# Optimization experiments

Hardware: AMD Instinct MI355X
Metric: run time of the kernel (lower is better)

Reference implementation:

```python
import jax, jax.numpy as jnp
import numpy as np


def setup_inputs() -> dict:
    key = jax.random.key(0)
    k1, k2 = jax.random.split(key)
    B, H, N, D = 4, 16, 2048, 64
    x = jax.random.normal(k1, (B, H, N, D), dtype=jnp.float32)
    wqkv = 0.02 * jax.random.normal(k2, (H, D, 3 * D), dtype=jnp.float32)
    bqkv = jnp.zeros((H, 1, 3 * D), dtype=jnp.float32)
    return {"x": x, "wqkv": wqkv, "bqkv": bqkv}


def reference(x, wqkv, bqkv):
    # x: [B, H, N, D]; wqkv: [H, D, 3D]; bqkv: [H, 1, 3D]
    B, H, N, D = x.shape
    scale = D ** (-0.5)
    qkv = jnp.einsum('bhnd,hde->bhne', x, wqkv) + bqkv  # [B,H,N,3D]
    # Faithful to torch: reshape (3D,) -> (D, 3) then unbind last axis,
    # i.e. q/k/v are interleaved (stride-3) columns of the projection.
    qkv = qkv.reshape(B, H, N, D, 3)
    q = qkv[..., 0] * scale
    k = qkv[..., 1]
    v = qkv[..., 2]
    attn = jnp.einsum('bhqd,bhkd->bhqk', q, k)  # [B,H,N,N]
    attn = jax.nn.softmax(attn, axis=-1)
    out = jnp.einsum('bhqk,bhkd->bhqd', attn, v)  # [B,H,N,D]
    return out
```

## Files before the change

kernel.cpp:

```cpp
#include <hip/hip_runtime.h>
#include <hip/hip_bf16.h>
#include <stdint.h>

typedef short bf16x8 __attribute__((ext_vector_type(8)));
typedef short bf16x4 __attribute__((ext_vector_type(4)));
typedef float f32x4 __attribute__((ext_vector_type(4)));

#define BHC 64
#define NQ 2048
#define DD 64
#define NE 192
#define LDP 72
#define QSCALE 0.1803368801111245f

__device__ __forceinline__ short f2bf(float f) {
  unsigned u = __float_as_uint(f);
  unsigned r = (u + 0x7FFFu + ((u >> 16) & 1u)) >> 16;
  return (short)r;
}

__device__ __forceinline__ bf16x8 pack8(float4 a, float4 b) {
  bf16x8 v;
  v[0] = f2bf(a.x); v[1] = f2bf(a.y); v[2] = f2bf(a.z); v[3] = f2bf(a.w);
  v[4] = f2bf(b.x); v[5] = f2bf(b.y); v[6] = f2bf(b.z); v[7] = f2bf(b.w);
  return v;
}

__device__ __forceinline__ short2 pk_bf16(float a, float b) {
  __hip_bfloat162 c = __float22bfloat162_rn(make_float2(a, b));
  return *reinterpret_cast<short2*>(&c);
}

__global__ __launch_bounds__(256) void wprep_kernel(
    const float* __restrict__ w, const float* __restrict__ bq,
    short* __restrict__ wp, float* __restrict__ biasp) {
  const int h = blockIdx.y;
  const int r = blockIdx.x * 256 + threadIdx.x;
  const int j = r & 7;
  const int t = r >> 3;
  const int quad = t & 3, col = (t >> 2) & 15;
  const int kc = (t >> 6) & 1, ntb = (t >> 7) & 3, wh = t >> 9;
  const int d = kc * 32 + quad * 8 + j;
  const int e = (ntb * 16 + col) * 3 + wh;
  wp[h * 12288 + r] = f2bf(w[((size_t)h * DD + d) * NE + e]);
  if (r < 192) {
    const int wh2 = r / 64, c = r - wh2 * 64;
    biasp[h * 192 + r] = bq[h * NE + c * 3 + wh2];
  }
}

__global__ __launch_bounds__(256, 4) void proj_kernel(
    const float* __restrict__ x, const short* __restrict__ wp,
    const float* __restrict__ biasp, short* __restrict__ Qg,
    short* __restrict__ Kg, short* __restrict__ Vtg) {
  __shared__ short sV[4][64 * 24];

  const int tid = threadIdx.x;
  const int bh = blockIdx.x >> 5;
  const int rb = blockIdx.x & 31;
  const int h = bh & 15;
  const int wave = tid >> 6;
  const int lane = tid & 63;
  const int col = lane & 15, quad = lane >> 4;
  const int row0 = rb * 64 + wave * 16;

  const float* xrow = x + ((size_t)bh * NQ + row0 + col) * DD;
  bf16x8 aq[2];
#pragma unroll
  for (int kc = 0; kc < 2; ++kc) {
    const float4* p4 = (const float4*)(xrow + kc * 32 + quad * 8);
    aq[kc] = pack8(p4[0], p4[1]);
  }

  const short* wph = wp + h * 12288;
  const int fo = (col * 4 + quad) * 8;

  f32x4 acc[12];
#pragma unroll
  for (int nt = 0; nt < 12; ++nt) acc[nt] = (f32x4){0.f, 0.f, 0.f, 0.f};

#pragma unroll
  for (int nt = 0; nt < 12; ++nt) {
    bf16x8 bw0 = *(const bf16x8*)(wph + (nt * 2 + 0) * 512 + fo);
    bf16x8 bw1 = *(const bf16x8*)(wph + (nt * 2 + 1) * 512 + fo);
    acc[nt] = __builtin_amdgcn_mfma_f32_16x16x32_bf16(bw0, aq[0], acc[nt], 0, 0, 0);
    acc[nt] = __builtin_amdgcn_mfma_f32_16x16x32_bf16(bw1, aq[1], acc[nt], 0, 0, 0);
  }

  const float* bph = biasp + h * 192;
  short* Qp = Qg + ((size_t)bh * NQ + row0 + col) * DD;
  short* Kp = Kg + ((size_t)bh * NQ + row0 + col) * DD;
  short* sVw = sV[wave];

#pragma unroll
  for (int nt = 0; nt < 12; ++nt) {
    const int wh = nt >> 2, ntb = nt & 3;
    const float4 b4 = *(const float4*)(bph + wh * 64 + ntb * 16 + quad * 4);
    float v0 = acc[nt][0] + b4.x, v1 = acc[nt][1] + b4.y;
    float v2 = acc[nt][2] + b4.z, v3 = acc[nt][3] + b4.w;
    if (nt < 4) { v0 *= QSCALE; v1 *= QSCALE; v2 *= QSCALE; v3 *= QSCALE; }
    if (nt < 8) {
      short2 s01 = pk_bf16(v0, v1);
      short2 s23 = pk_bf16(v2, v3);
      bf16x4 pv; pv[0] = s01.x; pv[1] = s01.y; pv[2] = s23.x; pv[3] = s23.y;
      short* P = (nt < 4) ? Qp : Kp;
      *(bf16x4*)(P + ntb * 16 + quad * 4) = pv;
    } else {
      const int dd = ntb * 16 + quad * 4;
      sVw[(dd + 0) * 24 + col] = f2bf(v0);
      sVw[(dd + 1) * 24 + col] = f2bf(v1);
      sVw[(dd + 2) * 24 + col] = f2bf(v2);
      sVw[(dd + 3) * 24 + col] = f2bf(v3);
    }
  }

  short* Vp = Vtg + (size_t)bh * DD * NQ + row0;
#pragma unroll
  for (int c = 0; c < 2; ++c) {
    int idx = c * 64 + lane;
    int d = idx >> 1, half = (idx & 1) * 8;
    *(bf16x8*)(Vp + (size_t)d * NQ + half) = *(const bf16x8*)(sVw + d * 24 + half);
  }
}

__global__ __launch_bounds__(256, 2) void attn_kernel(
    const short* __restrict__ Qg, const short* __restrict__ Kg,
    const short* __restrict__ Vtg, float* __restrict__ out) {
  __shared__ short kbuf[2][64 * 64];
  __shared__ short vbuf[2][64 * 64];
  __shared__ short pbuf[4][64 * LDP];

  const int tid = threadIdx.x;
  const int bh = blockIdx.x & 63;
  const int qb = blockIdx.x >> 6;
  const int wave = tid >> 6, lane = tid & 63;
  const int col = lane & 15, quad = lane >> 4;
  const int qbase = qb * 256 + wave * 64;

  bf16x8 bqf[4][2];
#pragma unroll
  for (int ntq = 0; ntq < 4; ++ntq)
#pragma unroll
    for (int kc = 0; kc < 2; ++kc)
      bqf[ntq][kc] = *(const bf16x8*)(Qg + ((size_t)bh * NQ + qbase + ntq * 16 + col) * DD +
                                      kc * 32 + quad * 8);

  f32x4 o[4][4];
  float l_acc[4];
#pragma unroll
  for (int mtq = 0; mtq < 4; ++mtq) {
    l_acc[mtq] = 0.f;
#pragma unroll
    for (int ntd = 0; ntd < 4; ++ntd) o[mtq][ntd] = (f32x4){0.f, 0.f, 0.f, 0.f};
  }

  short* pb = pbuf[wave];
  const short* Kb = Kg + (size_t)bh * NQ * DD;
  const short* Vb = Vtg + (size_t)bh * DD * NQ;

  const int r0 = tid >> 3, c0 = tid & 7;
  const int dst0 = r0 * 64 + ((c0 ^ (r0 & 7)) * 8);
  const int dst1 = (r0 + 32) * 64 + ((c0 ^ (r0 & 7)) * 8);
  const int src0 = r0 * DD + c0 * 8;
  const size_t vsrc0o = (size_t)r0 * NQ + c0 * 8;
  const size_t vsrc1o = (size_t)(r0 + 32) * NQ + c0 * 8;

  {
    bf16x8 k0 = *(const bf16x8*)(Kb + src0);
    bf16x8 k1 = *(const bf16x8*)(Kb + src0 + 32 * DD);
    bf16x8 v0 = *(const bf16x8*)(Vb + vsrc0o);
    bf16x8 v1 = *(const bf16x8*)(Vb + vsrc1o);
    *(bf16x8*)(&kbuf[0][dst0]) = k0;
    *(bf16x8*)(&kbuf[0][dst1]) = k1;
    *(bf16x8*)(&vbuf[0][dst0]) = v0;
    *(bf16x8*)(&vbuf[0][dst1]) = v1;
  }
  __syncthreads();

#pragma unroll 1
  for (int t = 0; t < 32; ++t) {
    const int p = t & 1;
    const short* kb = kbuf[p];
    const short* vb_s = vbuf[p];

    bf16x8 nk0, nk1, nv0, nv1;
    if (t < 31) {
      const short* Kn = Kb + (t + 1) * 64 * DD;
      const short* Vn = Vb + (t + 1) * 64;
      nk0 = *(const bf16x8*)(Kn + src0);
      nk1 = *(const bf16x8*)(Kn + src0 + 32 * DD);
      nv0 = *(const bf16x8*)(Vn + vsrc0o);
      nv1 = *(const bf16x8*)(Vn + vsrc1o);
    }

#pragma unroll
    for (int mtk = 0; mtk < 4; ++mtk) {
      const int krow = mtk * 16 + col;
      const int kx = krow & 7;
      bf16x8 ka0 = *(const bf16x8*)(&kb[krow * 64 + ((quad ^ kx) * 8)]);
      bf16x8 ka1 = *(const bf16x8*)(&kb[krow * 64 + (((4 + quad) ^ kx) * 8)]);
#pragma unroll
      for (int ntq = 0; ntq < 4; ++ntq) {
        f32x4 s = (f32x4){0.f, 0.f, 0.f, 0.f};
        s = __builtin_amdgcn_mfma_f32_16x16x32_bf16(ka0, bqf[ntq][0], s, 0, 0, 0);
        s = __builtin_amdgcn_mfma_f32_16x16x32_bf16(ka1, bqf[ntq][1], s, 0, 0, 0);
        float p0 = __builtin_amdgcn_exp2f(s[0]);
        float p1 = __builtin_amdgcn_exp2f(s[1]);
        float p2 = __builtin_amdgcn_exp2f(s[2]);
        float p3 = __builtin_amdgcn_exp2f(s[3]);
        l_acc[ntq] += (p0 + p1) + (p2 + p3);
        short2 s01 = pk_bf16(p0, p1);
        short2 s23 = pk_bf16(p2, p3);
        bf16x4 pv; pv[0] = s01.x; pv[1] = s01.y; pv[2] = s23.x; pv[3] = s23.y;
        *(bf16x4*)(&pb[(ntq * 16 + col) * LDP + mtk * 16 + quad * 4]) = pv;
      }
    }

#pragma unroll
    for (int mtq = 0; mtq < 4; ++mtq) {
      bf16x8 ap0 = *(const bf16x8*)(&pb[(mtq * 16 + col) * LDP + quad * 8]);
      bf16x8 ap1 = *(const bf16x8*)(&pb[(mtq * 16 + col) * LDP + 32 + quad * 8]);
#pragma unroll
      for (int ntd = 0; ntd < 4; ++ntd) {
        const int vrow = ntd * 16 + col;
        const int vx = vrow & 7;
        bf16x8 vf0 = *(const bf16x8*)(&vb_s[vrow * 64 + ((quad ^ vx) * 8)]);
        bf16x8 vf1 = *(const bf16x8*)(&vb_s[vrow * 64 + (((4 + quad) ^ vx) * 8)]);
        o[mtq][ntd] = __builtin_amdgcn_mfma_f32_16x16x32_bf16(ap0, vf0, o[mtq][ntd], 0, 0, 0);
        o[mtq][ntd] = __builtin_amdgcn_mfma_f32_16x16x32_bf16(ap1, vf1, o[mtq][ntd], 0, 0, 0);
      }
    }

    if (t < 31) {
      short* kn = kbuf[1 - p];
      short* vn = vbuf[1 - p];
      *(bf16x8*)(&kn[dst0]) = nk0;
      *(bf16x8*)(&kn[dst1]) = nk1;
      *(bf16x8*)(&vn[dst0]) = nv0;
      *(bf16x8*)(&vn[dst1]) = nv1;
      __syncthreads();
    }
  }

#pragma unroll
  for (int mtq = 0; mtq < 4; ++mtq) {
    float l = l_acc[mtq];
    l += __shfl_xor(l, 16);
    l += __shfl_xor(l, 32);
#pragma unroll
    for (int r = 0; r < 4; ++r) {
      float inv = 1.0f / __shfl(l, quad * 4 + r);
      int rq = qbase + mtq * 16 + quad * 4 + r;
      float* orow = out + ((size_t)bh * NQ + rq) * DD;
#pragma unroll
      for (int ntd = 0; ntd < 4; ++ntd) orow[ntd * 16 + col] = o[mtq][ntd][r] * inv;
    }
  }
}

extern "C" void kernel_launch(void* const* d_in, const int* in_sizes, int n_in,
                              void* d_out, int out_size, void* d_ws, size_t ws_size,
                              hipStream_t stream) {
  const float* x = (const float*)d_in[0];
  const float* w = (const float*)d_in[1];
  const float* bq = (const float*)d_in[2];
  float* out = (float*)d_out;

  short* Qg = (short*)d_ws;
  short* Kg = Qg + (size_t)BHC * NQ * DD;
  short* Vtg = Kg + (size_t)BHC * NQ * DD;
  short* wp = Vtg + (size_t)BHC * DD * NQ;
  float* biasp = (float*)(wp + 16 * 12288);

  wprep_kernel<<<dim3(48, 16), dim3(256), 0, stream>>>(w, bq, wp, biasp);
  proj_kernel<<<dim3(2048), dim3(256), 0, stream>>>(x, wp, biasp, Qg, Kg, Vtg);
  attn_kernel<<<dim3(512), dim3(256), 0, stream>>>(Qg, Kg, Vtg, out);
}
```

Before: 183.8 us.

## Hold projection weights in registers and loop each wave over four row tiles

The projection kernel now loads all 24 weight fragments into registers once per wave and reuses them across four 16-row tiles, so each wave covers 64 rows and the grid shrinks from 2048 to 512 blocks. The next tile's x rows are prefetched while the current tile's MFMAs run, and the bias is used as the initial accumulator. V is transposed through a wider shared tile so Vt stores are full 64-row contiguous chunks. This cuts repeated weight loads and per-block overhead, but raises register pressure and removes the occupancy hint from the launch bounds.

```diff
diff --git a/kernel.cpp b/kernel.cpp
--- a/kernel.cpp
+++ b/kernel.cpp
@@ -49,77 +49,95 @@
   }
 }
 
-__global__ __launch_bounds__(256, 4) void proj_kernel(
+__global__ __launch_bounds__(256) void proj_kernel(
     const float* __restrict__ x, const short* __restrict__ wp,
     const float* __restrict__ biasp, short* __restrict__ Qg,
     short* __restrict__ Kg, short* __restrict__ Vtg) {
-  __shared__ short sV[4][64 * 24];
+  __shared__ short sV[4][64 * 72];
 
   const int tid = threadIdx.x;
-  const int bh = blockIdx.x >> 5;
-  const int rb = blockIdx.x & 31;
+  const int bh = blockIdx.x >> 3;
+  const int rb = blockIdx.x & 7;
   const int h = bh & 15;
   const int wave = tid >> 6;
   const int lane = tid & 63;
   const int col = lane & 15, quad = lane >> 4;
-  const int row0 = rb * 64 + wave * 16;
-
-  const float* xrow = x + ((size_t)bh * NQ + row0 + col) * DD;
-  bf16x8 aq[2];
-#pragma unroll
-  for (int kc = 0; kc < 2; ++kc) {
-    const float4* p4 = (const float4*)(xrow + kc * 32 + quad * 8);
-    aq[kc] = pack8(p4[0], p4[1]);
-  }
+  const int wbase = rb * 256 + wave * 64;
 
   const short* wph = wp + h * 12288;
   const int fo = (col * 4 + quad) * 8;
-
-  f32x4 acc[12];
-#pragma unroll
-  for (int nt = 0; nt < 12; ++nt) acc[nt] = (f32x4){0.f, 0.f, 0.f, 0.f};
-
-#pragma unroll
-  for (int nt = 0; nt < 12; ++nt) {
-    bf16x8 bw0 = *(const bf16x8*)(wph + (nt * 2 + 0) * 512 + fo);
-    bf16x8 bw1 = *(const bf16x8*)(wph + (nt * 2 + 1) * 512 + fo);
-    acc[nt] = __builtin_amdgcn_mfma_f32_16x16x32_bf16(bw0, aq[0], acc[nt], 0, 0, 0);
-    acc[nt] = __builtin_amdgcn_mfma_f32_16x16x32_bf16(bw1, aq[1], acc[nt], 0, 0, 0);
-  }
+  bf16x8 wf[24];
+#pragma unroll
+  for (int i = 0; i < 24; ++i) wf[i] = *(const bf16x8*)(wph + i * 512 + fo);
 
   const float* bph = biasp + h * 192;
-  short* Qp = Qg + ((size_t)bh * NQ + row0 + col) * DD;
-  short* Kp = Kg + ((size_t)bh * NQ + row0 + col) * DD;
+  const float* xb = x + ((size_t)bh * NQ + wbase + col) * DD;
   short* sVw = sV[wave];
 
-#pragma unroll
-  for (int nt = 0; nt < 12; ++nt) {
-    const int wh = nt >> 2, ntb = nt & 3;
-    const float4 b4 = *(const float4*)(bph + wh * 64 + ntb * 16 + quad * 4);
-    float v0 = acc[nt][0] + b4.x, v1 = acc[nt][1] + b4.y;
-    float v2 = acc[nt][2] + b4.z, v3 = acc[nt][3] + b4.w;
-    if (nt < 4) { v0 *= QSCALE; v1 *= QSCALE; v2 *= QSCALE; v3 *= QSCALE; }
-    if (nt < 8) {
-      short2 s01 = pk_bf16(v0, v1);
-      short2 s23 = pk_bf16(v2, v3);
-      bf16x4 pv; pv[0] = s01.x; pv[1] = s01.y; pv[2] = s23.x; pv[3] = s23.y;
-      short* P = (nt < 4) ? Qp : Kp;
-      *(bf16x4*)(P + ntb * 16 + quad * 4) = pv;
-    } else {
-      const int dd = ntb * 16 + quad * 4;
-      sVw[(dd + 0) * 24 + col] = f2bf(v0);
-      sVw[(dd + 1) * 24 + col] = f2bf(v1);
-      sVw[(dd + 2) * 24 + col] = f2bf(v2);
-      sVw[(dd + 3) * 24 + col] = f2bf(v3);
-    }
-  }
-
-  short* Vp = Vtg + (size_t)bh * DD * NQ + row0;
-#pragma unroll
-  for (int c = 0; c < 2; ++c) {
-    int idx = c * 64 + lane;
-    int d = idx >> 1, half = (idx & 1) * 8;
-    *(bf16x8*)(Vp + (size_t)d * NQ + half) = *(const bf16x8*)(sVw + d * 24 + half);
+  bf16x8 aqc[2];
+#pragma unroll
+  for (int kc = 0; kc < 2; ++kc) {
+    const float4* p4 = (const float4*)(xb + kc * 32 + quad * 8);
+    aqc[kc] = pack8(p4[0], p4[1]);
+  }
+
+#pragma unroll
+  for (int r = 0; r < 4; ++r) {
+    float4 nx0, nx1, nx2, nx3;
+    if (r < 3) {
+      const float* xn = xb + (size_t)(r + 1) * 16 * DD;
+      nx0 = *(const float4*)(xn + quad * 8);
+      nx1 = *(const float4*)(xn + quad * 8 + 4);
+      nx2 = *(const float4*)(xn + 32 + quad * 8);
+      nx3 = *(const float4*)(xn + 32 + quad * 8 + 4);
+    }
+
+    f32x4 acc[12];
+#pragma unroll
+    for (int nt = 0; nt < 12; ++nt)
+      acc[nt] = *(const f32x4*)(bph + (nt >> 2) * 64 + (nt & 3) * 16 + quad * 4);
+
+#pragma unroll
+    for (int nt = 0; nt < 12; ++nt) {
+      acc[nt] = __builtin_amdgcn_mfma_f32_16x16x32_bf16(wf[nt * 2 + 0], aqc[0], acc[nt], 0, 0, 0);
+      acc[nt] = __builtin_amdgcn_mfma_f32_16x16x32_bf16(wf[nt * 2 + 1], aqc[1], acc[nt], 0, 0, 0);
+    }
+
+    short* Qp = Qg + ((size_t)bh * NQ + wbase + r * 16 + col) * DD;
+    short* Kp = Kg + ((size_t)bh * NQ + wbase + r * 16 + col) * DD;
+#pragma unroll
+    for (int nt = 0; nt < 12; ++nt) {
+      const int ntb = nt & 3;
+      float v0 = acc[nt][0], v1 = acc[nt][1], v2 = acc[nt][2], v3 = acc[nt][3];
+      if (nt < 4) { v0 *= QSCALE; v1 *= QSCALE; v2 *= QSCALE; v3 *= QSCALE; }
+      if (nt < 8) {
+        short2 s01 = pk_bf16(v0, v1);
+        short2 s23 = pk_bf16(v2, v3);
+        bf16x4 pv; pv[0] = s01.x; pv[1] = s01.y; pv[2] = s23.x; pv[3] = s23.y;
+        short* P = (nt < 4) ? Qp : Kp;
+        *(bf16x4*)(P + ntb * 16 + quad * 4) = pv;
+      } else {
+        const int dd = ntb * 16 + quad * 4;
+        const int rc = r * 16 + col;
+        sVw[(dd + 0) * 72 + rc] = f2bf(v0);
+        sVw[(dd + 1) * 72 + rc] = f2bf(v1);
+        sVw[(dd + 2) * 72 + rc] = f2bf(v2);
+        sVw[(dd + 3) * 72 + rc] = f2bf(v3);
+      }
+    }
+
+    if (r < 3) {
+      aqc[0] = pack8(nx0, nx1);
+      aqc[1] = pack8(nx2, nx3);
+    }
+  }
+
+  short* Vp = Vtg + (size_t)bh * DD * NQ + wbase;
+  const int dl = lane >> 3, ro = (lane & 7) * 8;
+#pragma unroll
+  for (int g = 0; g < 8; ++g) {
+    const int d = g * 8 + dl;
+    *(bf16x8*)(Vp + (size_t)d * NQ + ro) = *(const bf16x8*)(sVw + d * 72 + ro);
   }
 }
 
@@ -273,6 +291,6 @@
   float* biasp = (float*)(wp + 16 * 12288);
 
   wprep_kernel<<<dim3(48, 16), dim3(256), 0, stream>>>(w, bq, wp, biasp);
-  proj_kernel<<<dim3(2048), dim3(256), 0, stream>>>(x, wp, biasp, Qg, Kg, Vtg);
+  proj_kernel<<<dim3(512), dim3(256), 0, stream>>>(x, wp, biasp, Qg, Kg, Vtg);
   attn_kernel<<<dim3(512), dim3(256), 0, stream>>>(Qg, Kg, Vtg, out);
 }
```

New measurement: 181.6 us. About the same (-1.2%).
